# Kernel tuning notes

Hardware: AMD Instinct MI355X
Metric: run time of the kernel (lower is better)

Reference implementation:

```python
import jax, jax.numpy as jnp
import numpy as np

B = 256          # graphs per batch
NR = 268         # ROIs (nodes) per graph
N = B * NR       # total nodes
IC, OC = 256, 64 # in/out channels
NC = 7           # communities
DEG = 32
E = N * DEG      # total edges
K = int(NR * 0.8)  # 214 nodes kept per graph (floor, as torch .long())
LN_EPS = 1e-5


def setup_inputs() -> dict:
    key = jax.random.key(0)
    ks = jax.random.split(key, 10)
    x = jax.random.normal(ks[0], (N, IC), jnp.float32)
    # within-graph random edges: local src/dst in [0, NR) plus per-graph offset
    src = jax.random.randint(ks[1], (E,), 0, NR, dtype=jnp.int32)
    dst = jax.random.randint(ks[2], (E,), 0, NR, dtype=jnp.int32)
    off = jnp.repeat(jnp.arange(B, dtype=jnp.int32) * NR, NR * DEG)
    edge_index = jnp.stack([src + off, dst + off])  # (2, E)
    edge_attr = jax.random.uniform(ks[3], (E, 1), jnp.float32)
    batch = jnp.repeat(jnp.arange(B, dtype=jnp.int32), NR)
    xav = lambda k, shp: jax.random.normal(k, shp, jnp.float32) * np.float32(
        np.sqrt(2.0 / (shp[-2] + shp[-1])))
    return {
        "x": x, "edge_index": edge_index, "edge_attr": edge_attr, "batch": batch,
        "basis_kernels": xav(ks[4], (NC, IC, OC)),
        "roi_community": xav(ks[5], (NR, NC)),
        "ew_w": xav(ks[6], (1, OC)), "ew_b": jnp.zeros((OC,), jnp.float32),
        "conv_bias": jnp.zeros((OC,), jnp.float32),
        "ln_gamma": jnp.ones((OC,), jnp.float32), "ln_beta": jnp.zeros((OC,), jnp.float32),
        "att_w1": xav(ks[7], (OC, OC)), "att_b1": jnp.zeros((OC,), jnp.float32),
        "att_w2": xav(ks[8], (OC, 1)), "att_b2": jnp.zeros((1,), jnp.float32),
    }


def reference(x, edge_index, edge_attr, batch, basis_kernels, roi_community,
              ew_w, ew_b, conv_bias, ln_gamma, ln_beta,
              att_w1, att_b1, att_w2, att_b2):
    n = x.shape[0]
    loops = jnp.arange(n, dtype=edge_index.dtype)
    ei = jnp.concatenate([edge_index, jnp.stack([loops, loops])], axis=1)  # add self loops
    ea = jnp.concatenate([edge_attr, jnp.ones((n, 1), x.dtype)], axis=0)   # fill_value=1.0

    # ROI-aware kernels: per-node mixture of basis kernels
    cw = jax.nn.softmax(roi_community, axis=-1)            # (NR, NC)
    roi_k = jnp.einsum('rc,cio->rio', cw, basis_kernels)   # (NR, IC, OC)
    node_ids = loops % NR
    node_k = roi_k[node_ids]                               # (N, IC, OC) gather
    xt = jnp.einsum('ni,nio->no', x, node_k)               # per-node bmm

    # edge-gated message passing, scatter-add aggregation
    gate = jax.nn.sigmoid(ea @ ew_w + ew_b)                # (E+N, OC)
    msg = xt[ei[0]] * gate
    out = jax.ops.segment_sum(msg, ei[1], num_segments=n) + conv_bias

    out = jax.nn.elu(out)
    mu = jnp.mean(out, axis=-1, keepdims=True)
    var = jnp.mean(jnp.square(out - mu), axis=-1, keepdims=True)
    h = (out - mu) * jax.lax.rsqrt(var + LN_EPS) * ln_gamma + ln_beta
    # dropout: eval mode (identity)

    # R-pool: per-graph top-k (all graphs have NR contiguous nodes)
    scores = (jnp.tanh(h @ att_w1 + att_b1) @ att_w2 + att_b2).squeeze(-1)  # (N,)
    top_v, top_i = jax.lax.top_k(scores.reshape(B, NR), K)                  # (B, K)
    perm = (top_i.astype(jnp.int32) + jnp.arange(B, dtype=jnp.int32)[:, None] * NR).reshape(-1)
    x_pooled = h[perm] * jax.nn.sigmoid(top_v.reshape(-1))[:, None]
    batch_pooled = batch[perm]
    return x_pooled, batch_pooled, scores, perm
```

## Files before the change

### kernel.cpp

```cpp
#include <hip/hip_runtime.h>
#include <cstdint>
#include <cstddef>

#define NR   268
#define NB   256
#define NN   (NR*NB)
#define IC   256
#define OC   64
#define DEG  32
#define EPG  (NR*DEG)
#define NE   (NN*DEG)
#define KK   214

#define XP_OFF 0
#define BP_OFF 3506176
#define SC_OFF 3560960
#define PM_OFF 3629568

#define WS_ROIK 0
#define WS_XT   4390912
#define WS_META 8781824
#define WS_ROWS 13369344

#define PPG   4480
#define ZROW  (NR*OC)

typedef float v2f __attribute__((ext_vector_type(2)));

__device__ __forceinline__ v2f pkfma(v2f a, v2f b, v2f c) {
    v2f d;
    asm("v_pk_fma_f32 %0, %1, %2, %3" : "=v"(d) : "v"(a), "v"(b), "v"(c));
    return d;
}

#define NREP2 8
__global__ __launch_bounds__(1024, 2) void k_prep(const float* __restrict__ rc,
                                                  const float* __restrict__ basis,
                                                  float* __restrict__ roik,
                                                  const int* __restrict__ ei,
                                                  const float* __restrict__ ea,
                                                  float* __restrict__ meta,
                                                  unsigned int* __restrict__ rows) {
    __shared__ unsigned int cnt[NREP2][NR];
    __shared__ unsigned int tot[NR];
    __shared__ unsigned int prs[NR];
    __shared__ unsigned int pkb[PPG];
    __shared__ float daA[PPG];
    __shared__ float daB[PPG];
    int b = blockIdx.x;
    int tid = threadIdx.x;

    if (b >= NB) {
        int r = b - NB;
        float c[7];
        float m = -1e30f;
#pragma unroll
        for (int j = 0; j < 7; ++j) { c[j] = rc[r*7 + j]; m = fmaxf(m, c[j]); }
        float s = 0.f;
#pragma unroll
        for (int j = 0; j < 7; ++j) { c[j] = expf(c[j] - m); s += c[j]; }
        float inv = 1.f / s;
#pragma unroll
        for (int j = 0; j < 7; ++j) c[j] *= inv;
        for (int idx = tid; idx < IC*OC; idx += 1024) {
            float acc = 0.f;
#pragma unroll
            for (int j = 0; j < 7; ++j) acc = fmaf(c[j], basis[j*IC*OC + idx], acc);
            roik[(size_t)r*IC*OC + idx] = acc;
        }
        return;
    }

    int g = b;
    int wid = tid >> 7;
    for (int i = tid; i < NREP2*NR; i += 1024) ((unsigned*)cnt)[i] = 0u;
    for (int i = tid; i < PPG; i += 1024) pkb[i] = 0u;
    __syncthreads();
    int ebase = g * EPG;
    for (int e = tid; e < EPG; e += 1024) {
        int ld = ei[NE + ebase + e] - g * NR;
        atomicAdd(&cnt[wid][ld], 1u);
    }
    __syncthreads();
    for (int r = tid; r < NR; r += 1024) {
        unsigned t = 0;
#pragma unroll
        for (int s = 0; s < NREP2; ++s) t += cnt[s][r];
        tot[r] = t;
    }
    __syncthreads();
    if (tid < 64) {
        unsigned run = 0;
        for (int base = 0; base < NR; base += 64) {
            int idx = base + tid;
            unsigned v = (idx < NR) ? ((tot[idx] + 1u) >> 1) : 0u;
            unsigned orig = v;
#pragma unroll
            for (int s = 1; s < 64; s <<= 1) {
                int t = __shfl_up((int)v, (unsigned)s, 64);
                if (tid >= s) v += (unsigned)t;
            }
            if (idx < NR) prs[idx] = run + v - orig;
            run += (unsigned)__shfl((int)v, 63, 64);
        }
    }
    __syncthreads();
    for (int r = tid; r < NR; r += 1024) {
        unsigned base = 0;
#pragma unroll
        for (int s = 0; s < NREP2; ++s) { unsigned t = cnt[s][r]; cnt[s][r] = base; base += t; }
    }
    __syncthreads();
    unsigned lastPairs = (tot[NR-1] + 1u) >> 1;
    for (int i = tid; i < NR + 1; i += 1024)
        rows[(size_t)g * (NR + 1) + i] =
            (i < NR) ? prs[i] : (prs[NR-1] + lastPairs);
    for (int e = tid; e < EPG; e += 1024) {
        int src = ei[ebase + e] - g * NR;
        int ld  = ei[NE + ebase + e] - g * NR;
        float a = ea[ebase + e];
        unsigned rank = atomicAdd(&cnt[wid][ld], 1u);
        unsigned p = prs[ld] + (rank >> 1), sl = rank & 1u;
        atomicOr(&pkb[p], ((unsigned)src) << (16u * sl));
        if (sl) daB[p] = a - 0.5f; else daA[p] = a - 0.5f;
    }
    for (int r = tid; r < NR; r += 1024) {
        if (tot[r] & 1u) {
            unsigned p = prs[r] + (tot[r] >> 1);
            atomicOr(&pkb[p], 268u << 16);
            daB[p] = 0.f;
        }
    }
    __syncthreads();
    unsigned nPairs = prs[NR-1] + lastPairs;
    float4* __restrict__ mg = (float4*)(meta + (size_t)g * PPG * 4);
    for (unsigned i = tid; i < nPairs; i += 1024) {
        unsigned pk = pkb[i];
        float4 f;
        f.x = __int_as_float((int)(pk & 0xFFFFu) * OC);
        f.y = __int_as_float((int)(pk >> 16) * OC);
        f.z = daA[i];
        f.w = daB[i];
        mg[i] = f;
    }
}

#define GS3 130
__global__ __launch_bounds__(512) void k_xtf(const float* __restrict__ x,
                                             const float* __restrict__ roik,
                                             float* __restrict__ xt) {
    __shared__ __align__(16) float sXT[32 * GS3];
    __shared__ __align__(16) float sW[32 * OC];

    int bid = blockIdx.x;
    int r = bid % NR;
    int half = bid / NR;
    int tid = threadIdx.x;
    int lane = tid & 63;
    int wu = __builtin_amdgcn_readfirstlane(tid >> 6);
    int g0 = lane * 2;
    int o0 = wu * 8;

    const float* __restrict__ wk = roik + (size_t)r * (IC*OC);

    int quad = tid & 7, grp = tid >> 3;
    const float* __restrict__ xrowA =
        x + ((size_t)(half*128 + grp) * NR + r) * IC + quad*4;
    const float* __restrict__ xrowB = xrowA + (size_t)64 * NR * IC;

    float acc[2][8];
#pragma unroll
    for (int i = 0; i < 2; ++i)
#pragma unroll
        for (int j = 0; j < 8; ++j) acc[i][j] = 0.f;

    for (int kt = 0; kt < IC; kt += 32) {
        __syncthreads();
        {
            float4 xa = *(const float4*)(xrowA + kt);
            float4 xb = *(const float4*)(xrowB + kt);
            sXT[(quad*4+0)*GS3 + grp] = xa.x;
            sXT[(quad*4+1)*GS3 + grp] = xa.y;
            sXT[(quad*4+2)*GS3 + grp] = xa.z;
            sXT[(quad*4+3)*GS3 + grp] = xa.w;
            sXT[(quad*4+0)*GS3 + 64 + grp] = xb.x;
            sXT[(quad*4+1)*GS3 + 64 + grp] = xb.y;
            sXT[(quad*4+2)*GS3 + 64 + grp] = xb.z;
            sXT[(quad*4+3)*GS3 + 64 + grp] = xb.w;
            float4 wv = *(const float4*)(wk + (size_t)kt*OC + tid*4);
            *(float4*)(sW + tid*4) = wv;
        }
        __syncthreads();

#pragma unroll 8
        for (int k = 0; k < 32; ++k) {
            float2 xa = *(const float2*)&sXT[k*GS3 + g0];
            float4 wa = *(const float4*)&sW[k*OC + o0];
            float4 wb = *(const float4*)&sW[k*OC + o0 + 4];
            acc[0][0] = fmaf(xa.x, wa.x, acc[0][0]);
            acc[1][0] = fmaf(xa.y, wa.x, acc[1][0]);
            acc[0][1] = fmaf(xa.x, wa.y, acc[0][1]);
            acc[1][1] = fmaf(xa.y, wa.y, acc[1][1]);
            acc[0][2] = fmaf(xa.x, wa.z, acc[0][2]);
            acc[1][2] = fmaf(xa.y, wa.z, acc[1][2]);
            acc[0][3] = fmaf(xa.x, wa.w, acc[0][3]);
            acc[1][3] = fmaf(xa.y, wa.w, acc[1][3]);
            acc[0][4] = fmaf(xa.x, wb.x, acc[0][4]);
            acc[1][4] = fmaf(xa.y, wb.x, acc[1][4]);
            acc[0][5] = fmaf(xa.x, wb.y, acc[0][5]);
            acc[1][5] = fmaf(xa.y, wb.y, acc[1][5]);
            acc[0][6] = fmaf(xa.x, wb.z, acc[0][6]);
            acc[1][6] = fmaf(xa.y, wb.z, acc[1][6]);
            acc[0][7] = fmaf(xa.x, wb.w, acc[0][7]);
            acc[1][7] = fmaf(xa.y, wb.w, acc[1][7]);
        }
    }

#pragma unroll
    for (int i = 0; i < 2; ++i) {
        int g = half*128 + g0 + i;
        float* p = xt + ((size_t)g * NR + r) * OC + o0;
        float4 a; a.x = acc[i][0]; a.y = acc[i][1]; a.z = acc[i][2]; a.w = acc[i][3];
        float4 b; b.x = acc[i][4]; b.y = acc[i][5]; b.z = acc[i][6]; b.w = acc[i][7];
        *(float4*)p = a;
        *(float4*)(p + 4) = b;
    }
}

__global__ __launch_bounds__(1024, 4) void k_fused(
    const float* __restrict__ xt,
    const float4* __restrict__ meta,
    const unsigned int* __restrict__ rows,
    const float* __restrict__ ew_w, const float* __restrict__ ew_b,
    const float* __restrict__ conv_bias,
    const float* __restrict__ ln_g, const float* __restrict__ ln_b,
    const float* __restrict__ w1, const float* __restrict__ b1,
    const float* __restrict__ w2, const float* __restrict__ b2,
    float* __restrict__ out)
{
    extern __shared__ float smem[];
    float* xts = smem;
    float* hls = smem + (NR*OC + 64);
    __shared__ float rowbuf[16][OC];
    __shared__ float scl[NR];
    __shared__ int ord[KK];

    int g = blockIdx.x;
    int tid = threadIdx.x;
    int o = tid & 63, w = tid >> 6;

    {
        const float4* s4 = (const float4*)(xt + (size_t)g * NR * OC);
        float4* d4 = (float4*)xts;
        for (int i = tid; i < NR*OC/4; i += 1024) d4[i] = s4[i];
        if (tid < 16) d4[NR*OC/4 + tid] = make_float4(0.f, 0.f, 0.f, 0.f);
    }

    float wo = ew_w[o], bo = ew_b[o], cb = conv_bias[o];
    float lng = ln_g[o], lnb = ln_b[o];
    float w2o = w2[o], b1o = b1[o], b2s = b2[0];
    float sgself = 1.f / (1.f + expf(-(wo + bo)));

    float z0 = fmaf(0.5f, wo, bo);
    float sg0 = 1.f / (1.f + expf(-z0));
    float u  = sg0 * (1.f - sg0);
    float d2 = u * (1.f - 2.f*sg0);
    float d3 = u * (1.f - 6.f*u);
    float d4c = d2 * (1.f - 12.f*u);
    float k1 = u * wo;
    float k2 = d2 * wo*wo * 0.5f;
    float k3 = d3 * wo*wo*wo * (1.f/6.f);
    float k4 = d4c * wo*wo*wo*wo * (1.f/24.f);
    v2f kd4 = {k4, k4}, kd3 = {k3, k3}, kd2 = {k2, k2}, kd1 = {k1, k1};
    v2f sdv = {sg0, sg0};

    #define LOADW(j) \
        v2f wcA##j = { w1[(4*j+0)*OC+o], w1[(4*j+1)*OC+o] }; \
        v2f wcB##j = { w1[(4*j+2)*OC+o], w1[(4*j+3)*OC+o] };
    LOADW(0)  LOADW(1)  LOADW(2)  LOADW(3)
    LOADW(4)  LOADW(5)  LOADW(6)  LOADW(7)
    LOADW(8)  LOADW(9)  LOADW(10) LOADW(11)
    LOADW(12) LOADW(13) LOADW(14) LOADW(15)
    #undef LOADW

    const float4* __restrict__ gm = meta + (size_t)g * PPG;
    const unsigned int* __restrict__ gr = rows + (size_t)g * (NR + 1);
    const float* __restrict__ xo = xts + o;
    __syncthreads();

    #define PAIR(mp, acc) { \
        v2f xv; \
        xv.x = xo[__float_as_int((mp).x)]; \
        xv.y = xo[__float_as_int((mp).y)]; \
        v2f dv = { (mp).z, (mp).w }; \
        v2f t = pkfma(kd4, dv, kd3); \
        t = pkfma(t, dv, kd2); \
        t = pkfma(t, dv, kd1); \
        t = pkfma(t, dv, sdv); \
        acc = pkfma(xv, t, acc); }

    for (int r = w; r < NR; r += 16) {
        unsigned js = __builtin_amdgcn_readfirstlane(gr[r]);
        unsigned je = __builtin_amdgcn_readfirstlane(gr[r + 1]);
        v2f acc; acc.x = xts[r*OC + o] * sgself; acc.y = 0.f;
        unsigned j = js;
        for (; j + 8 <= je; j += 8) {
            float4 m0 = gm[j],   m1 = gm[j+1], m2 = gm[j+2], m3 = gm[j+3];
            float4 m4 = gm[j+4], m5 = gm[j+5], m6 = gm[j+6], m7 = gm[j+7];
            PAIR(m0, acc) PAIR(m1, acc) PAIR(m2, acc) PAIR(m3, acc)
            PAIR(m4, acc) PAIR(m5, acc) PAIR(m6, acc) PAIR(m7, acc)
        }
        if (j + 4 <= je) {
            float4 m0 = gm[j], m1 = gm[j+1], m2 = gm[j+2], m3 = gm[j+3];
            PAIR(m0, acc) PAIR(m1, acc) PAIR(m2, acc) PAIR(m3, acc)
            j += 4;
        }
        for (; j < je; ++j) {
            float4 m0 = gm[j];
            PAIR(m0, acc)
        }
        float accs = acc.x + acc.y + cb;
        float v = accs > 0.f ? accs : expm1f(accs);
        float s1 = v;
#pragma unroll
        for (int m = 1; m < 64; m <<= 1) s1 += __shfl_xor(s1, m, 64);
        float mu = s1 * (1.f/64.f);
        float d = v - mu;
        float s2 = d * d;
#pragma unroll
        for (int m = 1; m < 64; m <<= 1) s2 += __shfl_xor(s2, m, 64);
        float rsd = rsqrtf(s2 * (1.f/64.f) + 1e-5f);
        float h = fmaf(d * rsd, lng, lnb);
        hls[r*OC + o] = h;
        rowbuf[w][o] = h;
        {
            const float* hr = rowbuf[w];
            v2f tA = { b1o, 0.f }, tB = { 0.f, 0.f };
            #define STEP(j) { float4 h4 = *(const float4*)(hr + 4*j); \
                v2f hl = { h4.x, h4.y }, hh = { h4.z, h4.w }; \
                tA = pkfma(hl, wcA##j, tA); tB = pkfma(hh, wcB##j, tB); }
            STEP(0)  STEP(1)  STEP(2)  STEP(3)
            STEP(4)  STEP(5)  STEP(6)  STEP(7)
            STEP(8)  STEP(9)  STEP(10) STEP(11)
            STEP(12) STEP(13) STEP(14) STEP(15)
            #undef STEP
            float t = (tA.x + tA.y) + (tB.x + tB.y);
            float a2 = fminf(fmaxf(2.f * t, -80.f), 80.f);
            float y = expf(a2);
            float th = (y - 1.f) / (y + 1.f);
            float p = th * w2o;
#pragma unroll
            for (int m = 1; m < 64; m <<= 1) p += __shfl_xor(p, m, 64);
            if (o == 0) {
                float sc = p + b2s;
                scl[r] = sc;
                out[SC_OFF + (size_t)g * NR + r] = sc;
            }
        }
    }
    #undef PAIR
    __syncthreads();

    if (tid < NR) {
        float sr = scl[tid];
        int rank = 0;
        for (int jj = 0; jj < NR; ++jj) {
            float sj = scl[jj];
            rank += (sj > sr) || (sj == sr && jj < tid);
        }
        if (rank < KK) ord[rank] = tid;
    }
    __syncthreads();

    for (int k = w; k < KK; k += 16) {
        int r = ord[k];
        float v = scl[r];
        float gate = 1.f / (1.f + expf(-v));
        float hvv = hls[r*OC + o];
        out[XP_OFF + ((size_t)g*KK + k)*64 + o] = hvv * gate;
        if (o == 0) {
            out[BP_OFF + (size_t)g*KK + k] = (float)g;
            out[PM_OFF + (size_t)g*KK + k] = (float)(g*NR + r);
        }
    }
}

extern "C" void kernel_launch(void* const* d_in, const int* in_sizes, int n_in,
                              void* d_out, int out_size, void* d_ws, size_t ws_size,
                              hipStream_t stream) {
    const float* x     = (const float*)d_in[0];
    const int*   ei    = (const int*)d_in[1];
    const float* ea    = (const float*)d_in[2];
    const float* basis = (const float*)d_in[4];
    const float* rc    = (const float*)d_in[5];
    const float* ew_w  = (const float*)d_in[6];
    const float* ew_b  = (const float*)d_in[7];
    const float* cbias = (const float*)d_in[8];
    const float* ln_g  = (const float*)d_in[9];
    const float* ln_b  = (const float*)d_in[10];
    const float* w1    = (const float*)d_in[11];
    const float* b1    = (const float*)d_in[12];
    const float* w2    = (const float*)d_in[13];
    const float* b2    = (const float*)d_in[14];
    float* out = (float*)d_out;

    float* wsf = (float*)d_ws;
    float* roik = wsf + WS_ROIK;
    float* xtb  = wsf + WS_XT;
    float* metaF = wsf + WS_META;
    unsigned int* rows = (unsigned int*)(wsf + WS_ROWS);

    size_t fused_lds = (size_t)(NR*OC + 64 + NR*OC) * sizeof(float);

    k_prep <<<dim3(NB + NR), dim3(1024), 0, stream>>>(rc, basis, roik,
                                                      ei, ea, metaF, rows);
    k_xtf  <<<dim3(NR*2), dim3(512), 0, stream>>>(x, roik, xtb);
    k_fused<<<dim3(NB),   dim3(1024), fused_lds, stream>>>(
                                                  xtb, (const float4*)metaF, rows,
                                                  ew_w, ew_b, cbias, ln_g, ln_b,
                                                  w1, b1, w2, b2, out);
}
```

Baseline: 286.9 us.

## Merge CSR build and per-ROI transform into one front kernel, compute ROI kernels inline

Merges the prep kernel (softmax mixing of basis kernels into a per-ROI kernel buffer, plus per-graph CSR building) and the per-node transform kernel into a single launch. Blocks are interleaved so every third block builds one graph's CSR and the rest compute one ROI-half of the transform. The ROI kernel is no longer stored in the workspace: each transform block recomputes its mixed weights from the 7 basis kernels while staging weight tiles. This removes one launch, the inter-kernel dependency and the round trip of the materialised ROI kernel buffer. In exchange each transform block reads 7x more basis data per tile (mostly L2-resident) and uses a large dynamic LDS allocation that may limit occupancy.

Result: faster. 273.3 us (-4.7%).

```diff
diff --git a/kernel.cpp b/kernel.cpp
--- a/kernel.cpp
+++ b/kernel.cpp
@@ -17,7 +17,6 @@
 #define SC_OFF 3560960
 #define PM_OFF 3629568
 
-#define WS_ROIK 0
 #define WS_XT   4390912
 #define WS_META 8781824
 #define WS_ROWS 13369344
@@ -34,134 +33,128 @@
 }
 
 #define NREP2 8
-__global__ __launch_bounds__(1024, 2) void k_prep(const float* __restrict__ rc,
-                                                  const float* __restrict__ basis,
-                                                  float* __restrict__ roik,
-                                                  const int* __restrict__ ei,
-                                                  const float* __restrict__ ea,
-                                                  float* __restrict__ meta,
-                                                  unsigned int* __restrict__ rows) {
-    __shared__ unsigned int cnt[NREP2][NR];
-    __shared__ unsigned int tot[NR];
-    __shared__ unsigned int prs[NR];
-    __shared__ unsigned int pkb[PPG];
-    __shared__ float daA[PPG];
-    __shared__ float daB[PPG];
-    int b = blockIdx.x;
+#define GS3 130
+#define FRONT_LDS 64512
+__global__ __launch_bounds__(512) void k_front(const float* __restrict__ rc,
+                                               const float* __restrict__ basis,
+                                               const float* __restrict__ x,
+                                               float* __restrict__ xt,
+                                               const int* __restrict__ ei,
+                                               const float* __restrict__ ea,
+                                               float* __restrict__ meta,
+                                               unsigned int* __restrict__ rows) {
+    extern __shared__ __align__(16) unsigned char dynsm[];
+    int bid = blockIdx.x;
     int tid = threadIdx.x;
-
-    if (b >= NB) {
-        int r = b - NB;
-        float c[7];
-        float m = -1e30f;
-#pragma unroll
-        for (int j = 0; j < 7; ++j) { c[j] = rc[r*7 + j]; m = fmaxf(m, c[j]); }
-        float s = 0.f;
-#pragma unroll
-        for (int j = 0; j < 7; ++j) { c[j] = expf(c[j] - m); s += c[j]; }
-        float inv = 1.f / s;
-#pragma unroll
-        for (int j = 0; j < 7; ++j) c[j] *= inv;
-        for (int idx = tid; idx < IC*OC; idx += 1024) {
-            float acc = 0.f;
-#pragma unroll
-            for (int j = 0; j < 7; ++j) acc = fmaf(c[j], basis[j*IC*OC + idx], acc);
-            roik[(size_t)r*IC*OC + idx] = acc;
+    bool csr_role = (bid < 768) && (bid % 3 == 1);
+
+    if (csr_role) {
+        int g = bid / 3;
+        unsigned int* cnt = (unsigned int*)dynsm;
+        unsigned int* tot = cnt + NREP2*NR;
+        unsigned int* prs = tot + NR;
+        unsigned int* pkb = prs + NR;
+        float* daA = (float*)(pkb + PPG);
+        float* daB = daA + PPG;
+        int wid = tid >> 6;
+        for (int i = tid; i < NREP2*NR; i += 512) cnt[i] = 0u;
+        for (int i = tid; i < PPG; i += 512) pkb[i] = 0u;
+        __syncthreads();
+        int ebase = g * EPG;
+        for (int e = tid; e < EPG; e += 512) {
+            int ld = ei[NE + ebase + e] - g * NR;
+            atomicAdd(&cnt[wid*NR + ld], 1u);
+        }
+        __syncthreads();
+        for (int r = tid; r < NR; r += 512) {
+            unsigned t = 0;
+#pragma unroll
+            for (int s = 0; s < NREP2; ++s) t += cnt[s*NR + r];
+            tot[r] = t;
+        }
+        __syncthreads();
+        if (tid < 64) {
+            unsigned run = 0;
+            for (int base = 0; base < NR; base += 64) {
+                int idx = base + tid;
+                unsigned v = (idx < NR) ? ((tot[idx] + 1u) >> 1) : 0u;
+                unsigned orig = v;
+#pragma unroll
+                for (int s = 1; s < 64; s <<= 1) {
+                    int t = __shfl_up((int)v, (unsigned)s, 64);
+                    if (tid >= s) v += (unsigned)t;
+                }
+                if (idx < NR) prs[idx] = run + v - orig;
+                run += (unsigned)__shfl((int)v, 63, 64);
+            }
+        }
+        __syncthreads();
+        for (int r = tid; r < NR; r += 512) {
+            unsigned base = 0;
+#pragma unroll
+            for (int s = 0; s < NREP2; ++s) {
+                unsigned t = cnt[s*NR + r]; cnt[s*NR + r] = base; base += t;
+            }
+        }
+        __syncthreads();
+        unsigned lastPairs = (tot[NR-1] + 1u) >> 1;
+        for (int i = tid; i < NR + 1; i += 512)
+            rows[(size_t)g * (NR + 1) + i] =
+                (i < NR) ? prs[i] : (prs[NR-1] + lastPairs);
+        for (int e = tid; e < EPG; e += 512) {
+            int src = ei[ebase + e] - g * NR;
+            int ld  = ei[NE + ebase + e] - g * NR;
+            float a = ea[ebase + e];
+            unsigned rank = atomicAdd(&cnt[wid*NR + ld], 1u);
+            unsigned p = prs[ld] + (rank >> 1), sl = rank & 1u;
+            atomicOr(&pkb[p], ((unsigned)src) << (16u * sl));
+            if (sl) daB[p] = a - 0.5f; else daA[p] = a - 0.5f;
+        }
+        for (int r = tid; r < NR; r += 512) {
+            if (tot[r] & 1u) {
+                unsigned p = prs[r] + (tot[r] >> 1);
+                atomicOr(&pkb[p], 268u << 16);
+                daB[p] = 0.f;
+            }
+        }
+        __syncthreads();
+        unsigned nPairs = prs[NR-1] + lastPairs;
+        float4* __restrict__ mg = (float4*)(meta + (size_t)g * PPG * 4);
+        for (unsigned i = tid; i < nPairs; i += 512) {
+            unsigned pk = pkb[i];
+            float4 f;
+            f.x = __int_as_float((int)(pk & 0xFFFFu) * OC);
+            f.y = __int_as_float((int)(pk >> 16) * OC);
+            f.z = daA[i];
+            f.w = daB[i];
+            mg[i] = f;
         }
         return;
     }
 
-    int g = b;
-    int wid = tid >> 7;
-    for (int i = tid; i < NREP2*NR; i += 1024) ((unsigned*)cnt)[i] = 0u;
-    for (int i = tid; i < PPG; i += 1024) pkb[i] = 0u;
-    __syncthreads();
-    int ebase = g * EPG;
-    for (int e = tid; e < EPG; e += 1024) {
-        int ld = ei[NE + ebase + e] - g * NR;
-        atomicAdd(&cnt[wid][ld], 1u);
-    }
-    __syncthreads();
-    for (int r = tid; r < NR; r += 1024) {
-        unsigned t = 0;
-#pragma unroll
-        for (int s = 0; s < NREP2; ++s) t += cnt[s][r];
-        tot[r] = t;
-    }
-    __syncthreads();
-    if (tid < 64) {
-        unsigned run = 0;
-        for (int base = 0; base < NR; base += 64) {
-            int idx = base + tid;
-            unsigned v = (idx < NR) ? ((tot[idx] + 1u) >> 1) : 0u;
-            unsigned orig = v;
-#pragma unroll
-            for (int s = 1; s < 64; s <<= 1) {
-                int t = __shfl_up((int)v, (unsigned)s, 64);
-                if (tid >= s) v += (unsigned)t;
-            }
-            if (idx < NR) prs[idx] = run + v - orig;
-            run += (unsigned)__shfl((int)v, 63, 64);
-        }
-    }
-    __syncthreads();
-    for (int r = tid; r < NR; r += 1024) {
-        unsigned base = 0;
-#pragma unroll
-        for (int s = 0; s < NREP2; ++s) { unsigned t = cnt[s][r]; cnt[s][r] = base; base += t; }
-    }
-    __syncthreads();
-    unsigned lastPairs = (tot[NR-1] + 1u) >> 1;
-    for (int i = tid; i < NR + 1; i += 1024)
-        rows[(size_t)g * (NR + 1) + i] =
-            (i < NR) ? prs[i] : (prs[NR-1] + lastPairs);
-    for (int e = tid; e < EPG; e += 1024) {
-        int src = ei[ebase + e] - g * NR;
-        int ld  = ei[NE + ebase + e] - g * NR;
-        float a = ea[ebase + e];
-        unsigned rank = atomicAdd(&cnt[wid][ld], 1u);
-        unsigned p = prs[ld] + (rank >> 1), sl = rank & 1u;
-        atomicOr(&pkb[p], ((unsigned)src) << (16u * sl));
-        if (sl) daB[p] = a - 0.5f; else daA[p] = a - 0.5f;
-    }
-    for (int r = tid; r < NR; r += 1024) {
-        if (tot[r] & 1u) {
-            unsigned p = prs[r] + (tot[r] >> 1);
-            atomicOr(&pkb[p], 268u << 16);
-            daB[p] = 0.f;
-        }
-    }
-    __syncthreads();
-    unsigned nPairs = prs[NR-1] + lastPairs;
-    float4* __restrict__ mg = (float4*)(meta + (size_t)g * PPG * 4);
-    for (unsigned i = tid; i < nPairs; i += 1024) {
-        unsigned pk = pkb[i];
-        float4 f;
-        f.x = __int_as_float((int)(pk & 0xFFFFu) * OC);
-        f.y = __int_as_float((int)(pk >> 16) * OC);
-        f.z = daA[i];
-        f.w = daB[i];
-        mg[i] = f;
-    }
-}
-
-#define GS3 130
-__global__ __launch_bounds__(512) void k_xtf(const float* __restrict__ x,
-                                             const float* __restrict__ roik,
-                                             float* __restrict__ xt) {
-    __shared__ __align__(16) float sXT[32 * GS3];
-    __shared__ __align__(16) float sW[32 * OC];
-
-    int bid = blockIdx.x;
-    int r = bid % NR;
-    int half = bid / NR;
-    int tid = threadIdx.x;
+    int idx = bid - ((bid < 768) ? (bid + 2) / 3 : 256);
+    int r = idx % NR;
+    int half = idx / NR;
+    float* sXT = (float*)dynsm;
+    float* sW  = sXT + 32 * GS3;
+
     int lane = tid & 63;
     int wu = __builtin_amdgcn_readfirstlane(tid >> 6);
     int g0 = lane * 2;
     int o0 = wu * 8;
 
-    const float* __restrict__ wk = roik + (size_t)r * (IC*OC);
+    float cw[7];
+    {
+        float m = -1e30f;
+#pragma unroll
+        for (int j = 0; j < 7; ++j) { cw[j] = rc[r*7 + j]; m = fmaxf(m, cw[j]); }
+        float s = 0.f;
+#pragma unroll
+        for (int j = 0; j < 7; ++j) { cw[j] = expf(cw[j] - m); s += cw[j]; }
+        float inv = 1.f / s;
+#pragma unroll
+        for (int j = 0; j < 7; ++j) cw[j] *= inv;
+    }
 
     int quad = tid & 7, grp = tid >> 3;
     const float* __restrict__ xrowA =
@@ -187,8 +180,17 @@
             sXT[(quad*4+1)*GS3 + 64 + grp] = xb.y;
             sXT[(quad*4+2)*GS3 + 64 + grp] = xb.z;
             sXT[(quad*4+3)*GS3 + 64 + grp] = xb.w;
-            float4 wv = *(const float4*)(wk + (size_t)kt*OC + tid*4);
-            *(float4*)(sW + tid*4) = wv;
+            int e0 = kt*OC + tid*4;
+            float4 w4 = make_float4(0.f, 0.f, 0.f, 0.f);
+#pragma unroll
+            for (int j = 0; j < 7; ++j) {
+                float4 bv = *(const float4*)(basis + (size_t)j*IC*OC + e0);
+                w4.x = fmaf(cw[j], bv.x, w4.x);
+                w4.y = fmaf(cw[j], bv.y, w4.y);
+                w4.z = fmaf(cw[j], bv.z, w4.z);
+                w4.w = fmaf(cw[j], bv.w, w4.w);
+            }
+            *(float4*)(sW + tid*4) = w4;
         }
         __syncthreads();
 
@@ -405,17 +407,15 @@
     float* out = (float*)d_out;
 
     float* wsf = (float*)d_ws;
-    float* roik = wsf + WS_ROIK;
     float* xtb  = wsf + WS_XT;
     float* metaF = wsf + WS_META;
     unsigned int* rows = (unsigned int*)(wsf + WS_ROWS);
 
     size_t fused_lds = (size_t)(NR*OC + 64 + NR*OC) * sizeof(float);
 
-    k_prep <<<dim3(NB + NR), dim3(1024), 0, stream>>>(rc, basis, roik,
-                                                      ei, ea, metaF, rows);
-    k_xtf  <<<dim3(NR*2), dim3(512), 0, stream>>>(x, roik, xtb);
-    k_fused<<<dim3(NB),   dim3(1024), fused_lds, stream>>>(
+    k_front<<<dim3(792), dim3(512), FRONT_LDS, stream>>>(rc, basis, x, xtb,
+                                                         ei, ea, metaF, rows);
+    k_fused<<<dim3(NB),  dim3(1024), fused_lds, stream>>>(
                                                   xtb, (const float4*)metaF, rows,
                                                   ew_w, ew_b, cbias, ln_g, ln_b,
                                                   w1, b1, w2, b2, out);
```
